# Optimization experiments

Measured on AMD Instinct MI355X. Metric: run time of the kernel, lower is better.

The kernel has to match this reference:

```python
import jax, jax.numpy as jnp
import numpy as np

NEG = float(-2**32 + 1)  # mask fill value used by the original module
H = 8  # number of heads (matches init kwarg h)


def setup_inputs() -> dict:
    key = jax.random.key(0)
    B, S, D, Q, V = 4, 2048, 512, 64, 64
    ks = jax.random.split(key, 10)
    sc = 1.0 / np.sqrt(D)
    x = jax.random.normal(ks[0], (B, S, D), jnp.float32)
    padding_mask = jax.random.randint(ks[1], (B, S), 0, 2, jnp.int32)
    Wq = jax.random.normal(ks[2], (H * Q, D), jnp.float32) * sc
    bq = jnp.zeros((H * Q,), jnp.float32)
    Wk = jax.random.normal(ks[3], (H * Q, D), jnp.float32) * sc
    bk = jnp.zeros((H * Q,), jnp.float32)
    Wv = jax.random.normal(ks[4], (H * V, D), jnp.float32) * sc
    bv = jnp.zeros((H * V,), jnp.float32)
    Wo = jax.random.normal(ks[5], (D, H * V), jnp.float32) * (1.0 / np.sqrt(H * V))
    bo = jnp.zeros((D,), jnp.float32)
    return {"x": x, "padding_mask": padding_mask, "Wq": Wq, "bq": bq,
            "Wk": Wk, "bk": bk, "Wv": Wv, "bv": bv, "Wo": Wo, "bo": bo}


def reference(x, padding_mask, Wq, bq, Wk, bk, Wv, bv, Wo, bo):
    # stage is hardcoded to 'train' (mask=True in init), so the causal branch runs.
    B, S, D = x.shape
    q_dim = Wq.shape[0] // H
    v_dim = Wv.shape[0] // H

    def split_heads(t, d):
        # torch: cat(chunk(h, dim=-1), dim=0) -> head-major [H*B, S, d]
        return t.reshape(B, S, H, d).transpose(2, 0, 1, 3).reshape(H * B, S, d)

    Qh = split_heads(x @ Wq.T + bq, q_dim)   # [H*B, S, q]
    Kh = split_heads(x @ Wk.T + bk, q_dim)
    Vh = split_heads(x @ Wv.T + bv, v_dim)

    score = jnp.einsum('nsd,ntd->nst', Qh, Kh) / jnp.sqrt(jnp.float32(q_dim))  # [H*B,S,S]
    pre_score = score  # module returns the UNMASKED scores (saved before masking)

    # causal mask (mask=True, stage=='train')
    causal = jnp.tril(jnp.ones((S, S), jnp.float32))
    score = jnp.where(causal > 0, score, NEG)

    # padding mask: built batch-major [B*H,S,S] while score is head-major [H*B,...]
    # -- faithful reproduction of the original ordering quirk.
    pm = jnp.broadcast_to(padding_mask[:, None, None, :], (B, H, S, S)).reshape(B * H, S, S)
    score = jnp.where(pm == 0, NEG, score)

    attn = jax.nn.softmax(score, axis=-1)
    out = jnp.einsum('nst,ntd->nsd', attn, Vh)  # [H*B, S, v]

    # torch: cat(chunk(h, dim=0), dim=-1) -> [B, S, H*v]
    heads = out.reshape(H, B, S, v_dim).transpose(1, 2, 0, 3).reshape(B, S, H * v_dim)
    self_attention = heads @ Wo.T + bo
    return self_attention, pre_score
```

## Files before the change

kernel.cpp:

```cpp
#include <hip/hip_runtime.h>
#include <hip/hip_fp16.h>
#include <math.h>

typedef _Float16 f16;
typedef _Float16 f16x8 __attribute__((ext_vector_type(8)));
typedef _Float16 f16x4 __attribute__((ext_vector_type(4)));
typedef float    f32x4 __attribute__((ext_vector_type(4)));

#define MFMA16(a,b,c) __builtin_amdgcn_mfma_f32_16x16x32_f16(a, b, c, 0, 0, 0)

#define NEGV (-4294967296.0f)

__global__ __launch_bounds__(256) void qkv_gemm(
    const float* __restrict__ x,
    const float* __restrict__ Wq, const float* __restrict__ bq,
    const float* __restrict__ Wk, const float* __restrict__ bk,
    const float* __restrict__ Wv, const float* __restrict__ bv,
    f16* __restrict__ Qws, f16* __restrict__ Kws, f16* __restrict__ Vt)
{
    __shared__ f16 Al[128 * 48];
    __shared__ f16 Wl[64 * 48];

    const int tid = threadIdx.x;
    const int bx  = blockIdx.x;
    const int m0  = blockIdx.y * 128;
    const int widx = bx >> 3;
    const int n0   = (bx & 7) * 64;

    const float* W    = (widx == 0) ? Wq : (widx == 1) ? Wk : Wv;
    const float* bias = (widx == 0) ? bq : (widx == 1) ? bk : bv;

    const int wid = tid >> 6, lane = tid & 63;
    const int g = lane >> 4, c = lane & 15;
    const int wm = (wid >> 1) * 64, wn = (wid & 1) * 32;

    const int sr = tid >> 3, sc = tid & 7;

    f32x4 acc[4][2] = {};

    for (int kk = 0; kk < 512; kk += 32) {
        __syncthreads();
        #pragma unroll
        for (int rr = 0; rr < 4; ++rr) {
            int row = sr + rr * 32;
            float4 v = *(const float4*)&x[(size_t)(m0 + row) * 512 + kk + sc * 4];
            f16x4 h4 = {(f16)v.x, (f16)v.y, (f16)v.z, (f16)v.w};
            *(f16x4*)&Al[row * 48 + sc * 4] = h4;
        }
        #pragma unroll
        for (int rr = 0; rr < 2; ++rr) {
            int row = sr + rr * 32;
            float4 v = *(const float4*)&W[(size_t)(n0 + row) * 512 + kk + sc * 4];
            f16x4 h4 = {(f16)v.x, (f16)v.y, (f16)v.z, (f16)v.w};
            *(f16x4*)&Wl[row * 48 + sc * 4] = h4;
        }
        __syncthreads();

        f16x8 b0 = *(const f16x8*)&Wl[(wn +  0 + c) * 48 + g * 8];
        f16x8 b1 = *(const f16x8*)&Wl[(wn + 16 + c) * 48 + g * 8];
        #pragma unroll
        for (int mf = 0; mf < 4; ++mf) {
            f16x8 a = *(const f16x8*)&Al[(wm + mf * 16 + c) * 48 + g * 8];
            acc[mf][0] = MFMA16(a, b0, acc[mf][0]);
            acc[mf][1] = MFMA16(a, b1, acc[mf][1]);
        }
    }

    #pragma unroll
    for (int nf = 0; nf < 2; ++nf) {
        int cc = n0 + wn + nf * 16 + c;
        float bval = bias[cc];
        #pragma unroll
        for (int mf = 0; mf < 4; ++mf) {
            if (widx < 2) {
                f16* outp = (widx == 0) ? Qws : Kws;
                #pragma unroll
                for (int r = 0; r < 4; ++r) {
                    int mrow = m0 + wm + mf * 16 + g * 4 + r;
                    outp[(size_t)mrow * 512 + cc] = (f16)(acc[mf][nf][r] + bval);
                }
            } else {
                int h  = n0 >> 6;
                int d  = wn + nf * 16 + c;
                int t0 = m0 + wm + mf * 16 + g * 4;
                int b  = t0 >> 11;
                int ts = t0 & 2047;
                int nn = h * 4 + b;
                f16x4 pk = {(f16)(acc[mf][nf][0] + bval), (f16)(acc[mf][nf][1] + bval),
                            (f16)(acc[mf][nf][2] + bval), (f16)(acc[mf][nf][3] + bval)};
                *(f16x4*)&Vt[((size_t)(nn * 64 + d)) * 2048 + ts] = pk;
            }
        }
    }
}

__global__ __launch_bounds__(256) void attn_kernel(
    const f16* __restrict__ Qws, const f16* __restrict__ Kws,
    const f16* __restrict__ Vt,  const int* __restrict__ pmask,
    float* __restrict__ pre_score, f16* __restrict__ attn_out)
{
    __shared__ f16 Kl[64 * 72];
    __shared__ f16 Vl[64 * 72];
    __shared__ f16 Pl[4][32 * 72];

    const int tid = threadIdx.x;
    const int wid = tid >> 6, lane = tid & 63;
    const int g = lane >> 4, c = lane & 15;
    const int qt = blockIdx.x;
    const int n  = blockIdx.y;
    const int h = n >> 2, b = n & 3;
    const int pmrow = n >> 3;
    const int q0 = qt * 128 + wid * 32;

    f16x8 qf[2][2];
    #pragma unroll
    for (int mi = 0; mi < 2; ++mi)
        #pragma unroll
        for (int ks = 0; ks < 2; ++ks)
            qf[mi][ks] = *(const f16x8*)
                &Qws[(size_t)(b * 2048 + q0 + mi * 16 + c) * 512 + h * 64 + ks * 32 + g * 8];

    f32x4 o[2][4] = {};
    float mrow[2][4], lrow[2][4];
    #pragma unroll
    for (int mi = 0; mi < 2; ++mi)
        #pragma unroll
        for (int r = 0; r < 4; ++r) { mrow[mi][r] = -INFINITY; lrow[mi][r] = 0.0f; }

    const int sr = tid >> 3, sc = tid & 7;

    for (int kt = 0; kt < 32; ++kt) {
        __syncthreads();
        #pragma unroll
        for (int rr = 0; rr < 2; ++rr) {
            int row = sr + rr * 32;
            *(uint4*)&Kl[row * 72 + sc * 8] =
                *(const uint4*)&Kws[(size_t)(b * 2048 + kt * 64 + row) * 512 + h * 64 + sc * 8];
            *(uint4*)&Vl[row * 72 + sc * 8] =
                *(const uint4*)&Vt[(size_t)(n * 64 + row) * 2048 + kt * 64 + sc * 8];
        }
        __syncthreads();

        f32x4 s[2][4] = {};
        #pragma unroll
        for (int nf = 0; nf < 4; ++nf) {
            #pragma unroll
            for (int ks = 0; ks < 2; ++ks) {
                f16x8 kf = *(const f16x8*)&Kl[(nf * 16 + c) * 72 + ks * 32 + g * 8];
                s[0][nf] = MFMA16(qf[0][ks], kf, s[0][nf]);
                s[1][nf] = MFMA16(qf[1][ks], kf, s[1][nf]);
            }
        }

        #pragma unroll
        for (int nf = 0; nf < 4; ++nf) {
            int tg  = kt * 64 + nf * 16 + c;
            int pmv = pmask[pmrow * 2048 + tg];
            #pragma unroll
            for (int mi = 0; mi < 2; ++mi) {
                #pragma unroll
                for (int r = 0; r < 4; ++r) {
                    float v = s[mi][nf][r] * 0.125f;
                    int srow = qt * 128 + wid * 32 + mi * 16 + g * 4 + r;
                    __builtin_nontemporal_store(
                        v, &pre_score[((size_t)n * 2048 + srow) * 2048 + tg]);
                    s[mi][nf][r] = (tg <= srow && pmv != 0) ? v : NEGV;
                }
            }
        }

        float alpha[2][4];
        #pragma unroll
        for (int mi = 0; mi < 2; ++mi) {
            #pragma unroll
            for (int r = 0; r < 4; ++r) {
                float rm = fmaxf(fmaxf(s[mi][0][r], s[mi][1][r]),
                                 fmaxf(s[mi][2][r], s[mi][3][r]));
                rm = fmaxf(rm, __shfl_xor(rm, 1, 64));
                rm = fmaxf(rm, __shfl_xor(rm, 2, 64));
                rm = fmaxf(rm, __shfl_xor(rm, 4, 64));
                rm = fmaxf(rm, __shfl_xor(rm, 8, 64));
                float mn = fmaxf(mrow[mi][r], rm);
                alpha[mi][r] = __expf(mrow[mi][r] - mn);
                mrow[mi][r] = mn;
            }
        }
        #pragma unroll
        for (int mi = 0; mi < 2; ++mi) {
            float rs[4] = {0.f, 0.f, 0.f, 0.f};
            #pragma unroll
            for (int nf = 0; nf < 4; ++nf) {
                #pragma unroll
                for (int r = 0; r < 4; ++r) {
                    float p = __expf(s[mi][nf][r] - mrow[mi][r]);
                    rs[r] += p;
                    Pl[wid][(mi * 16 + g * 4 + r) * 72 + nf * 16 + c] = (f16)p;
                }
            }
            #pragma unroll
            for (int r = 0; r < 4; ++r) {
                float t = rs[r];
                t += __shfl_xor(t, 1, 64);
                t += __shfl_xor(t, 2, 64);
                t += __shfl_xor(t, 4, 64);
                t += __shfl_xor(t, 8, 64);
                lrow[mi][r] = lrow[mi][r] * alpha[mi][r] + t;
                #pragma unroll
                for (int dn = 0; dn < 4; ++dn) o[mi][dn][r] *= alpha[mi][r];
            }
        }
        __syncthreads();

        #pragma unroll
        for (int ks = 0; ks < 2; ++ks) {
            f16x8 pa0 = *(const f16x8*)&Pl[wid][( 0 + c) * 72 + ks * 32 + g * 8];
            f16x8 pa1 = *(const f16x8*)&Pl[wid][(16 + c) * 72 + ks * 32 + g * 8];
            #pragma unroll
            for (int dn = 0; dn < 4; ++dn) {
                f16x8 vb = *(const f16x8*)&Vl[(dn * 16 + c) * 72 + ks * 32 + g * 8];
                o[0][dn] = MFMA16(pa0, vb, o[0][dn]);
                o[1][dn] = MFMA16(pa1, vb, o[1][dn]);
            }
        }
    }

    #pragma unroll
    for (int mi = 0; mi < 2; ++mi)
        #pragma unroll
        for (int dn = 0; dn < 4; ++dn)
            #pragma unroll
            for (int r = 0; r < 4; ++r) {
                int srow = qt * 128 + wid * 32 + mi * 16 + g * 4 + r;
                attn_out[(size_t)(b * 2048 + srow) * 512 + h * 64 + dn * 16 + c] =
                    (f16)(o[mi][dn][r] / lrow[mi][r]);
            }
}

__global__ __launch_bounds__(256) void out_gemm(
    const f16* __restrict__ Aattn, const float* __restrict__ Wo,
    const float* __restrict__ bo, float* __restrict__ outp)
{
    __shared__ f16 Al[128 * 48];
    __shared__ f16 Wl[64 * 48];

    const int tid = threadIdx.x;
    const int n0 = blockIdx.x * 64;
    const int m0 = blockIdx.y * 128;
    const int wid = tid >> 6, lane = tid & 63;
    const int g = lane >> 4, c = lane & 15;
    const int wm = (wid >> 1) * 64, wn = (wid & 1) * 32;

    const int sr4 = tid >> 2, sc4 = tid & 3;
    const int sr8 = tid >> 3, sc8 = tid & 7;

    f32x4 acc[4][2] = {};

    for (int kk = 0; kk < 512; kk += 32) {
        __syncthreads();
        #pragma unroll
        for (int rr = 0; rr < 2; ++rr) {
            int row = sr4 + rr * 64;
            *(uint4*)&Al[row * 48 + sc4 * 8] =
                *(const uint4*)&Aattn[(size_t)(m0 + row) * 512 + kk + sc4 * 8];
        }
        #pragma unroll
        for (int rr = 0; rr < 2; ++rr) {
            int row = sr8 + rr * 32;
            float4 v = *(const float4*)&Wo[(size_t)(n0 + row) * 512 + kk + sc8 * 4];
            f16x4 h4 = {(f16)v.x, (f16)v.y, (f16)v.z, (f16)v.w};
            *(f16x4*)&Wl[row * 48 + sc8 * 4] = h4;
        }
        __syncthreads();

        f16x8 b0 = *(const f16x8*)&Wl[(wn +  0 + c) * 48 + g * 8];
        f16x8 b1 = *(const f16x8*)&Wl[(wn + 16 + c) * 48 + g * 8];
        #pragma unroll
        for (int mf = 0; mf < 4; ++mf) {
            f16x8 a = *(const f16x8*)&Al[(wm + mf * 16 + c) * 48 + g * 8];
            acc[mf][0] = MFMA16(a, b0, acc[mf][0]);
            acc[mf][1] = MFMA16(a, b1, acc[mf][1]);
        }
    }

    #pragma unroll
    for (int nf = 0; nf < 2; ++nf) {
        int cc = n0 + wn + nf * 16 + c;
        float bval = bo[cc];
        #pragma unroll
        for (int mf = 0; mf < 4; ++mf)
            #pragma unroll
            for (int r = 0; r < 4; ++r)
                outp[(size_t)(m0 + wm + mf * 16 + g * 4 + r) * 512 + cc] =
                    acc[mf][nf][r] + bval;
    }
}

extern "C" void kernel_launch(void* const* d_in, const int* in_sizes, int n_in,
                              void* d_out, int out_size, void* d_ws, size_t ws_size,
                              hipStream_t stream)
{
    (void)in_sizes; (void)n_in; (void)out_size; (void)ws_size;

    const float* x  = (const float*)d_in[0];
    const int*   pm = (const int*)  d_in[1];
    const float* Wq = (const float*)d_in[2];
    const float* bq = (const float*)d_in[3];
    const float* Wk = (const float*)d_in[4];
    const float* bk = (const float*)d_in[5];
    const float* Wv = (const float*)d_in[6];
    const float* bv = (const float*)d_in[7];
    const float* Wo = (const float*)d_in[8];
    const float* bo = (const float*)d_in[9];

    float* out = (float*)d_out;
    float* pre = out + (size_t)4 * 2048 * 512;

    f16* Qws  = (f16*)d_ws;
    f16* Kws  = Qws + (size_t)8192 * 512;
    f16* Vt   = Kws + (size_t)8192 * 512;
    f16* Aat  = Vt  + (size_t)2048 * 2048;

    qkv_gemm  <<<dim3(24, 64), 256, 0, stream>>>(x, Wq, bq, Wk, bk, Wv, bv, Qws, Kws, Vt);
    attn_kernel<<<dim3(16, 32), 256, 0, stream>>>(Qws, Kws, Vt, pm, pre, Aat);
    out_gemm  <<<dim3(8, 64),  256, 0, stream>>>(Aat, Wo, bo, out);
}
```

Before: 297.9 us.

## Skip causally masked softmax/PV tiles and shrink attention query tile

The attention kernel now uses 64-query blocks with 16 rows per wave, doubling the grid. For key tiles above the diagonal it only computes and writes the raw pre_score and skips masking, softmax, V loads and the PV MFMAs. Fully masked rows, whose output is the mean of V, are handled by a new vsum kernel that precomputes per-head V column sums. It also switches exp to exp2 with a folded log2e scale and replaces a block barrier with an LDS waitcnt, at the cost of an extra launch and more exact-match care for dead rows.

```diff
diff --git a/kernel.cpp b/kernel.cpp
--- a/kernel.cpp
+++ b/kernel.cpp
@@ -9,7 +9,8 @@
 
 #define MFMA16(a,b,c) __builtin_amdgcn_mfma_f32_16x16x32_f16(a, b, c, 0, 0, 0)
 
-#define NEGV (-4294967296.0f)
+#define MASKNEG (-6.0e9f)
+#define LOG2E   1.44269504088896f
 
 __global__ __launch_bounds__(256) void qkv_gemm(
     const float* __restrict__ x,
@@ -94,14 +95,33 @@
     }
 }
 
+__global__ __launch_bounds__(256) void vsum_kernel(
+    const f16* __restrict__ Vt, float* __restrict__ Vsum)
+{
+    const int row  = blockIdx.x * 4 + (threadIdx.x >> 6);
+    const int lane = threadIdx.x & 63;
+    const f16* p = Vt + (size_t)row * 2048;
+    float s = 0.f;
+    #pragma unroll
+    for (int i = 0; i < 4; ++i) {
+        f16x8 v = *(const f16x8*)&p[i * 512 + lane * 8];
+        #pragma unroll
+        for (int j = 0; j < 8; ++j) s += (float)v[j];
+    }
+    #pragma unroll
+    for (int off = 1; off < 64; off <<= 1) s += __shfl_xor(s, off, 64);
+    if (lane == 0) Vsum[row] = s;
+}
+
 __global__ __launch_bounds__(256) void attn_kernel(
     const f16* __restrict__ Qws, const f16* __restrict__ Kws,
     const f16* __restrict__ Vt,  const int* __restrict__ pmask,
+    const float* __restrict__ Vsum,
     float* __restrict__ pre_score, f16* __restrict__ attn_out)
 {
     __shared__ f16 Kl[64 * 72];
     __shared__ f16 Vl[64 * 72];
-    __shared__ f16 Pl[4][32 * 72];
+    __shared__ f16 Pl[4][16 * 72];
 
     const int tid = threadIdx.x;
     const int wid = tid >> 6, lane = tid & 63;
@@ -110,24 +130,22 @@
     const int n  = blockIdx.y;
     const int h = n >> 2, b = n & 3;
     const int pmrow = n >> 3;
-    const int q0 = qt * 128 + wid * 32;
-
-    f16x8 qf[2][2];
-    #pragma unroll
-    for (int mi = 0; mi < 2; ++mi)
-        #pragma unroll
-        for (int ks = 0; ks < 2; ++ks)
-            qf[mi][ks] = *(const f16x8*)
-                &Qws[(size_t)(b * 2048 + q0 + mi * 16 + c) * 512 + h * 64 + ks * 32 + g * 8];
-
-    f32x4 o[2][4] = {};
-    float mrow[2][4], lrow[2][4];
-    #pragma unroll
-    for (int mi = 0; mi < 2; ++mi)
-        #pragma unroll
-        for (int r = 0; r < 4; ++r) { mrow[mi][r] = -INFINITY; lrow[mi][r] = 0.0f; }
+    const int q0w = qt * 64 + wid * 16;
+
+    f16x8 qf[2];
+    #pragma unroll
+    for (int ks = 0; ks < 2; ++ks)
+        qf[ks] = *(const f16x8*)
+            &Qws[(size_t)(b * 2048 + q0w + c) * 512 + h * 64 + ks * 32 + g * 8];
+
+    f32x4 o[4] = {};
+    float mrow[4], lrow[4];
+    #pragma unroll
+    for (int r = 0; r < 4; ++r) { mrow[r] = -INFINITY; lrow[r] = 0.0f; }
 
     const int sr = tid >> 3, sc = tid & 7;
+    const int* pmp = pmask + pmrow * 2048;
+    float* prow = pre_score + ((size_t)n * 2048 + q0w + g * 4) * 2048;
 
     for (int kt = 0; kt < 32; ++kt) {
         __syncthreads();
@@ -136,67 +154,71 @@
             int row = sr + rr * 32;
             *(uint4*)&Kl[row * 72 + sc * 8] =
                 *(const uint4*)&Kws[(size_t)(b * 2048 + kt * 64 + row) * 512 + h * 64 + sc * 8];
-            *(uint4*)&Vl[row * 72 + sc * 8] =
-                *(const uint4*)&Vt[(size_t)(n * 64 + row) * 2048 + kt * 64 + sc * 8];
-        }
-        __syncthreads();
-
-        f32x4 s[2][4] = {};
+        }
+        if (kt <= qt) {
+            #pragma unroll
+            for (int rr = 0; rr < 2; ++rr) {
+                int row = sr + rr * 32;
+                *(uint4*)&Vl[row * 72 + sc * 8] =
+                    *(const uint4*)&Vt[(size_t)(n * 64 + row) * 2048 + kt * 64 + sc * 8];
+            }
+        }
+        __syncthreads();
+
+        f32x4 s[4] = {};
         #pragma unroll
         for (int nf = 0; nf < 4; ++nf) {
             #pragma unroll
             for (int ks = 0; ks < 2; ++ks) {
                 f16x8 kf = *(const f16x8*)&Kl[(nf * 16 + c) * 72 + ks * 32 + g * 8];
-                s[0][nf] = MFMA16(qf[0][ks], kf, s[0][nf]);
-                s[1][nf] = MFMA16(qf[1][ks], kf, s[1][nf]);
+                s[nf] = MFMA16(qf[ks], kf, s[nf]);
             }
         }
 
         #pragma unroll
         for (int nf = 0; nf < 4; ++nf) {
-            int tg  = kt * 64 + nf * 16 + c;
-            int pmv = pmask[pmrow * 2048 + tg];
-            #pragma unroll
-            for (int mi = 0; mi < 2; ++mi) {
+            int tg = kt * 64 + nf * 16 + c;
+            #pragma unroll
+            for (int r = 0; r < 4; ++r)
+                __builtin_nontemporal_store(s[nf][r] * 0.125f,
+                                            &prow[(size_t)r * 2048 + tg]);
+        }
+
+        if (kt <= qt) {
+            float sl[4][4];
+            #pragma unroll
+            for (int nf = 0; nf < 4; ++nf) {
+                int tg  = kt * 64 + nf * 16 + c;
+                int pmv = pmp[tg];
                 #pragma unroll
                 for (int r = 0; r < 4; ++r) {
-                    float v = s[mi][nf][r] * 0.125f;
-                    int srow = qt * 128 + wid * 32 + mi * 16 + g * 4 + r;
-                    __builtin_nontemporal_store(
-                        v, &pre_score[((size_t)n * 2048 + srow) * 2048 + tg]);
-                    s[mi][nf][r] = (tg <= srow && pmv != 0) ? v : NEGV;
+                    int srow = q0w + g * 4 + r;
+                    sl[nf][r] = (tg <= srow && pmv != 0)
+                              ? s[nf][r] * (0.125f * LOG2E) : MASKNEG;
                 }
             }
-        }
-
-        float alpha[2][4];
-        #pragma unroll
-        for (int mi = 0; mi < 2; ++mi) {
+            float alpha[4];
             #pragma unroll
             for (int r = 0; r < 4; ++r) {
-                float rm = fmaxf(fmaxf(s[mi][0][r], s[mi][1][r]),
-                                 fmaxf(s[mi][2][r], s[mi][3][r]));
+                float rm = fmaxf(fmaxf(sl[0][r], sl[1][r]),
+                                 fmaxf(sl[2][r], sl[3][r]));
                 rm = fmaxf(rm, __shfl_xor(rm, 1, 64));
                 rm = fmaxf(rm, __shfl_xor(rm, 2, 64));
                 rm = fmaxf(rm, __shfl_xor(rm, 4, 64));
                 rm = fmaxf(rm, __shfl_xor(rm, 8, 64));
-                float mn = fmaxf(mrow[mi][r], rm);
-                alpha[mi][r] = __expf(mrow[mi][r] - mn);
-                mrow[mi][r] = mn;
-            }
-        }
-        #pragma unroll
-        for (int mi = 0; mi < 2; ++mi) {
+                float mn = fmaxf(mrow[r], rm);
+                alpha[r] = exp2f(mrow[r] - mn);
+                mrow[r] = mn;
+            }
             float rs[4] = {0.f, 0.f, 0.f, 0.f};
             #pragma unroll
-            for (int nf = 0; nf < 4; ++nf) {
+            for (int nf = 0; nf < 4; ++nf)
                 #pragma unroll
                 for (int r = 0; r < 4; ++r) {
-                    float p = __expf(s[mi][nf][r] - mrow[mi][r]);
+                    float p = exp2f(sl[nf][r] - mrow[r]);
                     rs[r] += p;
-                    Pl[wid][(mi * 16 + g * 4 + r) * 72 + nf * 16 + c] = (f16)p;
+                    Pl[wid][(g * 4 + r) * 72 + nf * 16 + c] = (f16)p;
                 }
-            }
             #pragma unroll
             for (int r = 0; r < 4; ++r) {
                 float t = rs[r];
@@ -204,36 +226,36 @@
                 t += __shfl_xor(t, 2, 64);
                 t += __shfl_xor(t, 4, 64);
                 t += __shfl_xor(t, 8, 64);
-                lrow[mi][r] = lrow[mi][r] * alpha[mi][r] + t;
-                #pragma unroll
-                for (int dn = 0; dn < 4; ++dn) o[mi][dn][r] *= alpha[mi][r];
-            }
-        }
-        __syncthreads();
-
-        #pragma unroll
-        for (int ks = 0; ks < 2; ++ks) {
-            f16x8 pa0 = *(const f16x8*)&Pl[wid][( 0 + c) * 72 + ks * 32 + g * 8];
-            f16x8 pa1 = *(const f16x8*)&Pl[wid][(16 + c) * 72 + ks * 32 + g * 8];
-            #pragma unroll
-            for (int dn = 0; dn < 4; ++dn) {
-                f16x8 vb = *(const f16x8*)&Vl[(dn * 16 + c) * 72 + ks * 32 + g * 8];
-                o[0][dn] = MFMA16(pa0, vb, o[0][dn]);
-                o[1][dn] = MFMA16(pa1, vb, o[1][dn]);
-            }
-        }
-    }
-
-    #pragma unroll
-    for (int mi = 0; mi < 2; ++mi)
-        #pragma unroll
-        for (int dn = 0; dn < 4; ++dn)
-            #pragma unroll
-            for (int r = 0; r < 4; ++r) {
-                int srow = qt * 128 + wid * 32 + mi * 16 + g * 4 + r;
-                attn_out[(size_t)(b * 2048 + srow) * 512 + h * 64 + dn * 16 + c] =
-                    (f16)(o[mi][dn][r] / lrow[mi][r]);
-            }
+                lrow[r] = lrow[r] * alpha[r] + t;
+                #pragma unroll
+                for (int dn = 0; dn < 4; ++dn) o[dn][r] *= alpha[r];
+            }
+            asm volatile("s_waitcnt lgkmcnt(0)" ::: "memory");
+
+            #pragma unroll
+            for (int ks = 0; ks < 2; ++ks) {
+                f16x8 pa = *(const f16x8*)&Pl[wid][c * 72 + ks * 32 + g * 8];
+                #pragma unroll
+                for (int dn = 0; dn < 4; ++dn) {
+                    f16x8 vb = *(const f16x8*)&Vl[(dn * 16 + c) * 72 + ks * 32 + g * 8];
+                    o[dn] = MFMA16(pa, vb, o[dn]);
+                }
+            }
+        }
+    }
+
+    #pragma unroll
+    for (int r = 0; r < 4; ++r) {
+        int srow = q0w + g * 4 + r;
+        bool dead = (mrow[r] == MASKNEG);
+        float inv_l = dead ? 0.f : 1.0f / lrow[r];
+        #pragma unroll
+        for (int dn = 0; dn < 4; ++dn) {
+            float val = dead ? Vsum[n * 64 + dn * 16 + c] * (1.0f / 2048.0f)
+                             : o[dn][r] * inv_l;
+            attn_out[(size_t)(b * 2048 + srow) * 512 + h * 64 + dn * 16 + c] = (f16)val;
+        }
+    }
 }
 
 __global__ __launch_bounds__(256) void out_gemm(
@@ -315,12 +337,14 @@
     float* out = (float*)d_out;
     float* pre = out + (size_t)4 * 2048 * 512;
 
-    f16* Qws  = (f16*)d_ws;
-    f16* Kws  = Qws + (size_t)8192 * 512;
-    f16* Vt   = Kws + (size_t)8192 * 512;
-    f16* Aat  = Vt  + (size_t)2048 * 2048;
-
-    qkv_gemm  <<<dim3(24, 64), 256, 0, stream>>>(x, Wq, bq, Wk, bk, Wv, bv, Qws, Kws, Vt);
-    attn_kernel<<<dim3(16, 32), 256, 0, stream>>>(Qws, Kws, Vt, pm, pre, Aat);
-    out_gemm  <<<dim3(8, 64),  256, 0, stream>>>(Aat, Wo, bo, out);
-}
+    f16*   Qws  = (f16*)d_ws;
+    f16*   Kws  = Qws + (size_t)8192 * 512;
+    f16*   Vt   = Kws + (size_t)8192 * 512;
+    f16*   Aat  = Vt  + (size_t)2048 * 2048;
+    float* Vsum = (float*)(Aat + (size_t)8192 * 512);
+
+    qkv_gemm   <<<dim3(24, 64), 256, 0, stream>>>(x, Wq, bq, Wk, bk, Wv, bv, Qws, Kws, Vt);
+    vsum_kernel<<<dim3(512),    256, 0, stream>>>(Vt, Vsum);
+    attn_kernel<<<dim3(32, 32), 256, 0, stream>>>(Qws, Kws, Vt, pm, Vsum, pre, Aat);
+    out_gemm   <<<dim3(8, 64),  256, 0, stream>>>(Aat, Wo, bo, out);
+}
```

Result: slower. 323.5 us (+8.6%).

## Skip softmax/PV work on causally masked key tiles, handle fully-masked rows via V mean

Applied to the files above, without the earlier changes.

The attention loop runs the full softmax and PV update only for key tiles at or below the diagonal. Above the diagonal it only computes QK to write the unmasked pre_score output. Rows where every key is masked (all-padding) take the mean of V, precomputed by a new vsum kernel, to match the uniform softmax the reference produces. The change also switches to exp2 with log2e prescaling and replaces a block barrier with a waitcnt on the per-wave P buffer; the exact-equality test against the mask constant for dead rows is a fragile edge case.

```diff
diff --git a/kernel.cpp b/kernel.cpp
--- a/kernel.cpp
+++ b/kernel.cpp
@@ -9,7 +9,8 @@
 
 #define MFMA16(a,b,c) __builtin_amdgcn_mfma_f32_16x16x32_f16(a, b, c, 0, 0, 0)
 
-#define NEGV (-4294967296.0f)
+#define MASKNEG (-6.0e9f)
+#define LOG2E   1.44269504088896f
 
 __global__ __launch_bounds__(256) void qkv_gemm(
     const float* __restrict__ x,
@@ -94,9 +95,28 @@
     }
 }
 
+__global__ __launch_bounds__(256) void vsum_kernel(
+    const f16* __restrict__ Vt, float* __restrict__ Vsum)
+{
+    const int row  = blockIdx.x * 4 + (threadIdx.x >> 6);
+    const int lane = threadIdx.x & 63;
+    const f16* p = Vt + (size_t)row * 2048;
+    float s = 0.f;
+    #pragma unroll
+    for (int i = 0; i < 4; ++i) {
+        f16x8 v = *(const f16x8*)&p[i * 512 + lane * 8];
+        #pragma unroll
+        for (int j = 0; j < 8; ++j) s += (float)v[j];
+    }
+    #pragma unroll
+    for (int off = 1; off < 64; off <<= 1) s += __shfl_xor(s, off, 64);
+    if (lane == 0) Vsum[row] = s;
+}
+
 __global__ __launch_bounds__(256) void attn_kernel(
     const f16* __restrict__ Qws, const f16* __restrict__ Kws,
     const f16* __restrict__ Vt,  const int* __restrict__ pmask,
+    const float* __restrict__ Vsum,
     float* __restrict__ pre_score, f16* __restrict__ attn_out)
 {
     __shared__ f16 Kl[64 * 72];
@@ -111,6 +131,7 @@
     const int h = n >> 2, b = n & 3;
     const int pmrow = n >> 3;
     const int q0 = qt * 128 + wid * 32;
+    const int live = 2 * qt + 2;
 
     f16x8 qf[2][2];
     #pragma unroll
@@ -128,50 +149,51 @@
         for (int r = 0; r < 4; ++r) { mrow[mi][r] = -INFINITY; lrow[mi][r] = 0.0f; }
 
     const int sr = tid >> 3, sc = tid & 7;
-
-    for (int kt = 0; kt < 32; ++kt) {
+    const int* pmp = pmask + pmrow * 2048;
+    const f16* Kbase = Kws + (size_t)(b * 2048) * 512 + h * 64;
+    const f16* Vbase = Vt + (size_t)(n * 64) * 2048;
+
+    for (int kt = 0; kt < live; ++kt) {
         __syncthreads();
         #pragma unroll
         for (int rr = 0; rr < 2; ++rr) {
             int row = sr + rr * 32;
             *(uint4*)&Kl[row * 72 + sc * 8] =
-                *(const uint4*)&Kws[(size_t)(b * 2048 + kt * 64 + row) * 512 + h * 64 + sc * 8];
+                *(const uint4*)&Kbase[(size_t)(kt * 64 + row) * 512 + sc * 8];
             *(uint4*)&Vl[row * 72 + sc * 8] =
-                *(const uint4*)&Vt[(size_t)(n * 64 + row) * 2048 + kt * 64 + sc * 8];
+                *(const uint4*)&Vbase[(size_t)row * 2048 + kt * 64 + sc * 8];
         }
         __syncthreads();
 
         f32x4 s[2][4] = {};
         #pragma unroll
-        for (int nf = 0; nf < 4; ++nf) {
+        for (int nf = 0; nf < 4; ++nf)
             #pragma unroll
             for (int ks = 0; ks < 2; ++ks) {
                 f16x8 kf = *(const f16x8*)&Kl[(nf * 16 + c) * 72 + ks * 32 + g * 8];
                 s[0][nf] = MFMA16(qf[0][ks], kf, s[0][nf]);
                 s[1][nf] = MFMA16(qf[1][ks], kf, s[1][nf]);
             }
-        }
 
         #pragma unroll
         for (int nf = 0; nf < 4; ++nf) {
             int tg  = kt * 64 + nf * 16 + c;
-            int pmv = pmask[pmrow * 2048 + tg];
-            #pragma unroll
-            for (int mi = 0; mi < 2; ++mi) {
+            int pmv = pmp[tg];
+            #pragma unroll
+            for (int mi = 0; mi < 2; ++mi)
                 #pragma unroll
                 for (int r = 0; r < 4; ++r) {
                     float v = s[mi][nf][r] * 0.125f;
-                    int srow = qt * 128 + wid * 32 + mi * 16 + g * 4 + r;
+                    int srow = q0 + mi * 16 + g * 4 + r;
                     __builtin_nontemporal_store(
                         v, &pre_score[((size_t)n * 2048 + srow) * 2048 + tg]);
-                    s[mi][nf][r] = (tg <= srow && pmv != 0) ? v : NEGV;
+                    s[mi][nf][r] = (tg <= srow && pmv != 0) ? v * LOG2E : MASKNEG;
                 }
-            }
         }
 
         float alpha[2][4];
         #pragma unroll
-        for (int mi = 0; mi < 2; ++mi) {
+        for (int mi = 0; mi < 2; ++mi)
             #pragma unroll
             for (int r = 0; r < 4; ++r) {
                 float rm = fmaxf(fmaxf(s[mi][0][r], s[mi][1][r]),
@@ -181,22 +203,20 @@
                 rm = fmaxf(rm, __shfl_xor(rm, 4, 64));
                 rm = fmaxf(rm, __shfl_xor(rm, 8, 64));
                 float mn = fmaxf(mrow[mi][r], rm);
-                alpha[mi][r] = __expf(mrow[mi][r] - mn);
+                alpha[mi][r] = exp2f(mrow[mi][r] - mn);
                 mrow[mi][r] = mn;
             }
-        }
         #pragma unroll
         for (int mi = 0; mi < 2; ++mi) {
             float rs[4] = {0.f, 0.f, 0.f, 0.f};
             #pragma unroll
-            for (int nf = 0; nf < 4; ++nf) {
+            for (int nf = 0; nf < 4; ++nf)
                 #pragma unroll
                 for (int r = 0; r < 4; ++r) {
-                    float p = __expf(s[mi][nf][r] - mrow[mi][r]);
+                    float p = exp2f(s[mi][nf][r] - mrow[mi][r]);
                     rs[r] += p;
                     Pl[wid][(mi * 16 + g * 4 + r) * 72 + nf * 16 + c] = (f16)p;
                 }
-            }
             #pragma unroll
             for (int r = 0; r < 4; ++r) {
                 float t = rs[r];
@@ -209,7 +229,7 @@
                 for (int dn = 0; dn < 4; ++dn) o[mi][dn][r] *= alpha[mi][r];
             }
         }
-        __syncthreads();
+        asm volatile("s_waitcnt lgkmcnt(0)" ::: "memory");
 
         #pragma unroll
         for (int ks = 0; ks < 2; ++ks) {
@@ -224,16 +244,53 @@
         }
     }
 
+    for (int kt = live; kt < 32; ++kt) {
+        __syncthreads();
+        #pragma unroll
+        for (int rr = 0; rr < 2; ++rr) {
+            int row = sr + rr * 32;
+            *(uint4*)&Kl[row * 72 + sc * 8] =
+                *(const uint4*)&Kbase[(size_t)(kt * 64 + row) * 512 + sc * 8];
+        }
+        __syncthreads();
+
+        f32x4 s[2][4] = {};
+        #pragma unroll
+        for (int nf = 0; nf < 4; ++nf)
+            #pragma unroll
+            for (int ks = 0; ks < 2; ++ks) {
+                f16x8 kf = *(const f16x8*)&Kl[(nf * 16 + c) * 72 + ks * 32 + g * 8];
+                s[0][nf] = MFMA16(qf[0][ks], kf, s[0][nf]);
+                s[1][nf] = MFMA16(qf[1][ks], kf, s[1][nf]);
+            }
+        #pragma unroll
+        for (int nf = 0; nf < 4; ++nf) {
+            int tg = kt * 64 + nf * 16 + c;
+            #pragma unroll
+            for (int mi = 0; mi < 2; ++mi)
+                #pragma unroll
+                for (int r = 0; r < 4; ++r) {
+                    int srow = q0 + mi * 16 + g * 4 + r;
+                    __builtin_nontemporal_store(s[mi][nf][r] * 0.125f,
+                        &pre_score[((size_t)n * 2048 + srow) * 2048 + tg]);
+                }
+        }
+    }
+
     #pragma unroll
     for (int mi = 0; mi < 2; ++mi)
         #pragma unroll
-        for (int dn = 0; dn < 4; ++dn)
-            #pragma unroll
-            for (int r = 0; r < 4; ++r) {
-                int srow = qt * 128 + wid * 32 + mi * 16 + g * 4 + r;
-                attn_out[(size_t)(b * 2048 + srow) * 512 + h * 64 + dn * 16 + c] =
-                    (f16)(o[mi][dn][r] / lrow[mi][r]);
-            }
+        for (int r = 0; r < 4; ++r) {
+            int srow = q0 + mi * 16 + g * 4 + r;
+            bool dead = (mrow[mi][r] == MASKNEG);
+            float inv_l = dead ? 0.f : 1.0f / lrow[mi][r];
+            #pragma unroll
+            for (int dn = 0; dn < 4; ++dn) {
+                float val = dead ? Vsum[n * 64 + dn * 16 + c] * (1.0f / 2048.0f)
+                                 : o[mi][dn][r] * inv_l;
+                attn_out[(size_t)(b * 2048 + srow) * 512 + h * 64 + dn * 16 + c] = (f16)val;
+            }
+        }
 }
 
 __global__ __launch_bounds__(256) void out_gemm(
@@ -315,12 +372,14 @@
     float* out = (float*)d_out;
     float* pre = out + (size_t)4 * 2048 * 512;
 
-    f16* Qws  = (f16*)d_ws;
-    f16* Kws  = Qws + (size_t)8192 * 512;
-    f16* Vt   = Kws + (size_t)8192 * 512;
-    f16* Aat  = Vt  + (size_t)2048 * 2048;
-
-    qkv_gemm  <<<dim3(24, 64), 256, 0, stream>>>(x, Wq, bq, Wk, bk, Wv, bv, Qws, Kws, Vt);
-    attn_kernel<<<dim3(16, 32), 256, 0, stream>>>(Qws, Kws, Vt, pm, pre, Aat);
-    out_gemm  <<<dim3(8, 64),  256, 0, stream>>>(Aat, Wo, bo, out);
-}
+    f16*   Qws  = (f16*)d_ws;
+    f16*   Kws  = Qws + (size_t)8192 * 512;
+    f16*   Vt   = Kws + (size_t)8192 * 512;
+    f16*   Aat  = Vt  + (size_t)2048 * 2048;
+    float* Vsum = (float*)(Aat + (size_t)8192 * 512);
+
+    qkv_gemm   <<<dim3(24, 64), 256, 0, stream>>>(x, Wq, bq, Wk, bk, Wv, bv, Qws, Kws, Vt);
+    vsum_kernel<<<dim3(512),    256, 0, stream>>>(Vt, Vsum);
+    attn_kernel<<<dim3(16, 32), 256, 0, stream>>>(Qws, Kws, Vt, pm, Vsum, pre, Aat);
+    out_gemm   <<<dim3(8, 64),  256, 0, stream>>>(Aat, Wo, bo, out);
+}
```

Result: slower. 337.0 us (+13.2%).
